# Optimization experiments

Measured on AMD Instinct MI355X. Metric: run time of the kernel, lower is better.

## Reference

```python
import jax, jax.numpy as jnp
import numpy as np

N = 4_194_304        # total nodes in the batch
NUM_GRAPHS = 32_768  # number of graphs (segments)
VOCAB = 100          # Embedding(100, 1)

# Wigner-3j contraction constants (real basis)
C01 = float(1.0 / np.sqrt(3.0))   # 0e x 1e -> 1e and 1e x 0e -> 1e
C11 = float(1.0 / np.sqrt(6.0))   # 1e x 1e -> 1e (Levi-Civita / sqrt(6))
# path weights: sqrt(ir_out.dim / fan_in_paths); 3 paths -> 1.0, 2 paths -> sqrt(3/2)
PW1 = 1.0
PW2 = float(np.sqrt(1.5))


def setup_inputs() -> dict:
    key = jax.random.key(0)
    ks = jax.random.split(key, 12)
    z = jax.random.randint(ks[0], (N,), 0, VOCAB, dtype=jnp.int32)
    pos = jax.random.normal(ks[1], (N, 3), dtype=jnp.float32)
    batch = jnp.sort(jax.random.randint(ks[2], (N,), 0, NUM_GRAPHS, dtype=jnp.int32))
    embed_table = jax.random.normal(ks[3], (VOCAB, 1), dtype=jnp.float32)
    lin_w = jax.random.normal(ks[4], (3, 3), dtype=jnp.float32) / np.sqrt(3.0)
    lin_b = jax.random.normal(ks[5], (3,), dtype=jnp.float32) * 0.1
    tp1_w = jax.random.normal(ks[6], (3,), dtype=jnp.float32)   # 3 CG paths
    tp2_w = jax.random.normal(ks[7], (2,), dtype=jnp.float32)   # 2 CG paths
    tp3_w = jax.random.normal(ks[8], (2,), dtype=jnp.float32)
    gate_w = jax.random.normal(ks[9], (2,), dtype=jnp.float32)
    fc_w = jax.random.normal(ks[10], (3, 3), dtype=jnp.float32) / np.sqrt(3.0)
    fc_b = jax.random.normal(ks[11], (3,), dtype=jnp.float32) * 0.1
    return {"z": z, "pos": pos, "batch": batch, "embed_table": embed_table,
            "lin_w": lin_w, "lin_b": lin_b, "tp1_w": tp1_w, "tp2_w": tp2_w,
            "tp3_w": tp3_w, "gate_w": gate_w, "fc_w": fc_w, "fc_b": fc_b}


def reference(z, pos, batch, embed_table, lin_w, lin_b, tp1_w, tp2_w, tp3_w, gate_w, fc_w, fc_b):
    # node features: x = [scalar embedding s (0e), transformed position v (1e)]
    s = embed_table[z][:, 0]                      # [N]
    v = pos @ lin_w.T + lin_b                     # [N, 3]
    sv = s[:, None] * v                           # [N, 3]

    # layer 1: FullyConnectedTP(x, x -> 1e); paths (0e,1e), (1e,0e), (1e,1e)
    # note: cross(v, v) == 0 structurally, kept for faithfulness to the module
    out = PW1 * (tp1_w[0] * C01 * sv
                 + tp1_w[1] * C01 * sv
                 + tp1_w[2] * C11 * jnp.cross(v, v))

    # layers 2, 3 and gate: FullyConnectedTP(out (1e), x (0e+1e) -> 1e)
    for w in (tp2_w, tp3_w, gate_w):
        out = PW2 * (w[0] * C01 * out * s[:, None]
                     + w[1] * C11 * jnp.cross(out, v))

    out = out @ fc_w.T + fc_b                     # [N, 3]
    return jax.ops.segment_sum(out, batch, num_segments=NUM_GRAPHS)  # [G, 3]
```

## Files before the change

### kernel.cpp

```cpp
#include <hip/hip_runtime.h>

#define BLOCK 256
#define NPT 8
#define CHUNK (BLOCK * NPT)
#define TBL 64

__global__ __launch_bounds__(BLOCK) void e3nn_one(
    const int* __restrict__ z, const float* __restrict__ pos,
    const int* __restrict__ batch, const float* __restrict__ embed,
    const float* __restrict__ lin_w, const float* __restrict__ lin_b,
    const float* __restrict__ tp1_w, const float* __restrict__ tp2_w,
    const float* __restrict__ tp3_w, const float* __restrict__ gate_w,
    const float* __restrict__ fc_w, const float* __restrict__ fc_b,
    float* __restrict__ out, int n, int G)
{
    __shared__ float t4[100];
    __shared__ float acc[TBL * 5];

    const int tid  = threadIdx.x;
    const int lane = tid & 63;
    const int b    = blockIdx.x;
    const int s    = b * CHUNK;
    const int e    = min(s + CHUNK, n);

    if (tid < 100) { float v = embed[tid]; float v2 = v * v; t4[tid] = v2 * v2; }
    for (int i = tid; i < TBL * 5; i += BLOCK) acc[i] = 0.f;
    __syncthreads();

    const int prev   = (s == 0) ? -1 : batch[s - 1];
    const int mylast = batch[e - 1];

    const long long i0 = (long long)s + (long long)tid * NPT;
    float px[NPT], py[NPT], pz[NPT];
    int zi[NPT], bi[NPT];

    if (i0 + NPT <= (long long)n) {
        const float4* p4 = (const float4*)(pos + i0 * 3);
        float4 q0 = p4[0], q1 = p4[1], q2 = p4[2], q3 = p4[3], q4 = p4[4], q5 = p4[5];
        px[0]=q0.x; py[0]=q0.y; pz[0]=q0.z;
        px[1]=q0.w; py[1]=q1.x; pz[1]=q1.y;
        px[2]=q1.z; py[2]=q1.w; pz[2]=q2.x;
        px[3]=q2.y; py[3]=q2.z; pz[3]=q2.w;
        px[4]=q3.x; py[4]=q3.y; pz[4]=q3.z;
        px[5]=q3.w; py[5]=q4.x; pz[5]=q4.y;
        px[6]=q4.z; py[6]=q4.w; pz[6]=q5.x;
        px[7]=q5.y; py[7]=q5.z; pz[7]=q5.w;
        int4 za = *(const int4*)(z + i0), zb = *(const int4*)(z + i0 + 4);
        zi[0]=za.x; zi[1]=za.y; zi[2]=za.z; zi[3]=za.w;
        zi[4]=zb.x; zi[5]=zb.y; zi[6]=zb.z; zi[7]=zb.w;
        int4 ba = *(const int4*)(batch + i0), bb = *(const int4*)(batch + i0 + 4);
        bi[0]=ba.x; bi[1]=ba.y; bi[2]=ba.z; bi[3]=ba.w;
        bi[4]=bb.x; bi[5]=bb.y; bi[6]=bb.z; bi[7]=bb.w;
    } else {
#pragma unroll
        for (int k = 0; k < NPT; ++k) {
            long long i = i0 + k;
            if (i < (long long)n) {
                px[k]=pos[i*3]; py[k]=pos[i*3+1]; pz[k]=pos[i*3+2];
                zi[k]=z[i]; bi[k]=batch[i];
            } else { px[k]=0.f; py[k]=0.f; pz[k]=0.f; zi[k]=0; bi[k]=-1; }
        }
    }

    auto lflush = [&](int g, float ax, float ay, float az, float at, float ac) {
        int slot = g - prev - 1;
        if (slot >= 0 && slot < TBL) {
            atomicAdd(&acc[slot*5+0], ax);
            atomicAdd(&acc[slot*5+1], ay);
            atomicAdd(&acc[slot*5+2], az);
            atomicAdd(&acc[slot*5+3], at);
            atomicAdd(&acc[slot*5+4], ac);
        }
    };

    float ax=0.f, ay=0.f, az=0.f, at=0.f, ac=0.f;
    int rb = -1;
#pragma unroll
    for (int k = 0; k < NPT; ++k) {
        if (bi[k] < 0) continue;
        float t = t4[zi[k]];
        if (bi[k] == rb) {
            ax += t*px[k]; ay += t*py[k]; az += t*pz[k]; at += t; ac += 1.f;
        } else {
            if (rb >= 0) lflush(rb, ax, ay, az, at, ac);
            rb = bi[k];
            ax = t*px[k]; ay = t*py[k]; az = t*pz[k]; at = t; ac = 1.f;
        }
    }

#pragma unroll
    for (int off = 1; off < 64; off <<= 1) {
        int   ob = __shfl_down(rb, off);
        float qx = __shfl_down(ax, off);
        float qy = __shfl_down(ay, off);
        float qz = __shfl_down(az, off);
        float qt = __shfl_down(at, off);
        float qc = __shfl_down(ac, off);
        if ((lane + off) < 64 && ob == rb) {
            ax += qx; ay += qy; az += qz; at += qt; ac += qc;
        }
    }
    {
        int pb = __shfl_up(rb, 1);
        bool head = (lane == 0) || (pb != rb);
        if (rb >= 0 && head) lflush(rb, ax, ay, az, at, ac);
    }

    if ((tid >> 6) == 3 && e < n && mylast > prev) {
        float sx=0.f, sy=0.f, sz=0.f, st=0.f, sc=0.f;
        int base = e;
        for (;;) {
            bool allok = true;
#pragma unroll
            for (int k = 0; k < 4; ++k) {
                int idx = base + lane * 4 + k;
                bool ok = (idx < n) && (batch[idx] == mylast);
                if (ok) {
                    float t = t4[z[idx]];
                    sx += t*pos[3*idx]; sy += t*pos[3*idx+1]; sz += t*pos[3*idx+2];
                    st += t; sc += 1.f;
                } else allok = false;
            }
            unsigned long long m = __ballot(allok);
            if (m != ~0ULL) break;
            base += 256;
        }
#pragma unroll
        for (int off = 1; off < 64; off <<= 1) {
            sx += __shfl_xor(sx, off);
            sy += __shfl_xor(sy, off);
            sz += __shfl_xor(sz, off);
            st += __shfl_xor(st, off);
            sc += __shfl_xor(sc, off);
        }
        if (lane == 0) {
            int slot = mylast - prev - 1;
            if (slot < TBL) {
                atomicAdd(&acc[slot*5+0], sx);
                atomicAdd(&acc[slot*5+1], sy);
                atomicAdd(&acc[slot*5+2], sz);
                atomicAdd(&acc[slot*5+3], st);
                atomicAdd(&acc[slot*5+4], sc);
            }
        }
    }

    __syncthreads();

    const float C01 = 0.57735026918962576f;
    const float PW2 = 1.2247448713915890f;
    const float k1  = (tp1_w[0] + tp1_w[1]) * C01;
    const float C   = k1 * (PW2*tp2_w[0]*C01) * (PW2*tp3_w[0]*C01) * (PW2*gate_w[0]*C01);

    float lw[9], fw[9], lbv[3], fbv[3];
#pragma unroll
    for (int i = 0; i < 9; ++i) { lw[i] = lin_w[i]; fw[i] = fc_w[i]; }
#pragma unroll
    for (int i = 0; i < 3; ++i) { lbv[i] = lin_b[i]; fbv[i] = fc_b[i]; }

    float W[9], u[3];
#pragma unroll
    for (int r = 0; r < 3; ++r) {
#pragma unroll
        for (int cc = 0; cc < 3; ++cc)
            W[r*3+cc] = fw[r*3+0]*lw[0*3+cc] + fw[r*3+1]*lw[1*3+cc] + fw[r*3+2]*lw[2*3+cc];
        u[r] = fw[r*3+0]*lbv[0] + fw[r*3+1]*lbv[1] + fw[r*3+2]*lbv[2];
    }

    const int gend  = (e == n) ? (G - 1) : mylast;
    const int count = gend - prev;

    for (int o = tid; o < count; o += BLOCK) {
        float vx=0.f, vy=0.f, vz=0.f, vt=0.f, vc=0.f;
        if (o < TBL) {
            vx = acc[o*5+0]; vy = acc[o*5+1]; vz = acc[o*5+2];
            vt = acc[o*5+3]; vc = acc[o*5+4];
        }
        int g = prev + 1 + o;
        out[3*g+0] = C * (W[0]*vx + W[1]*vy + W[2]*vz + vt*u[0]) + vc*fbv[0];
        out[3*g+1] = C * (W[3]*vx + W[4]*vy + W[5]*vz + vt*u[1]) + vc*fbv[1];
        out[3*g+2] = C * (W[6]*vx + W[7]*vy + W[8]*vz + vt*u[2]) + vc*fbv[2];
    }
}

extern "C" void kernel_launch(void* const* d_in, const int* in_sizes, int n_in,
                              void* d_out, int out_size, void* d_ws, size_t ws_size,
                              hipStream_t stream) {
    const int*   z     = (const int*)  d_in[0];
    const float* pos   = (const float*)d_in[1];
    const int*   batch = (const int*)  d_in[2];
    const float* embed = (const float*)d_in[3];
    const float* lin_w = (const float*)d_in[4];
    const float* lin_b = (const float*)d_in[5];
    const float* tp1_w = (const float*)d_in[6];
    const float* tp2_w = (const float*)d_in[7];
    const float* tp3_w = (const float*)d_in[8];
    const float* gate_w= (const float*)d_in[9];
    const float* fc_w  = (const float*)d_in[10];
    const float* fc_b  = (const float*)d_in[11];
    float* out = (float*)d_out;

    int n = in_sizes[0];
    int G = out_size / 3;

    int nblocks = (n + CHUNK - 1) / CHUNK;
    e3nn_one<<<nblocks, BLOCK, 0, stream>>>(
        z, pos, batch, embed, lin_w, lin_b,
        tp1_w, tp2_w, tp3_w, gate_w, fc_w, fc_b, out, n, G);
}
```

Before: 22.54 us.

## Stage node loads through padded shared memory for fully coalesced global reads

Full chunks now load pos, z and batch with lane-contiguous float4/int4 reads (stride across threads) and transpose them through a bank-padded shared-memory buffer, so each thread still gets its 8 consecutive nodes. The embedding lookup t4[z] is done during staging, and the global loads are issued before the table/accumulator init to overlap latency. The aim is to replace the per-thread strided 96-byte vector loads with coalesced accesses. In exchange it adds about 25KB of shared memory per block (lower occupancy) and three extra barriers.

```diff
diff --git a/kernel.cpp b/kernel.cpp
--- a/kernel.cpp
+++ b/kernel.cpp
@@ -4,6 +4,8 @@
 #define NPT 8
 #define CHUNK (BLOCK * NPT)
 #define TBL 64
+
+__device__ __forceinline__ int padw(int w) { return w + (w >> 5); }
 
 __global__ __launch_bounds__(BLOCK) void e3nn_one(
     const int* __restrict__ z, const float* __restrict__ pos,
@@ -14,8 +16,9 @@
     const float* __restrict__ fc_w, const float* __restrict__ fc_b,
     float* __restrict__ out, int n, int G)
 {
-    __shared__ float t4[100];
+    __shared__ float t4s[100];
     __shared__ float acc[TBL * 5];
+    __shared__ float stage[6336];
 
     const int tid  = threadIdx.x;
     const int lane = tid & 63;
@@ -23,42 +26,89 @@
     const int s    = b * CHUNK;
     const int e    = min(s + CHUNK, n);
 
-    if (tid < 100) { float v = embed[tid]; float v2 = v * v; t4[tid] = v2 * v2; }
-    for (int i = tid; i < TBL * 5; i += BLOCK) acc[i] = 0.f;
-    __syncthreads();
-
     const int prev   = (s == 0) ? -1 : batch[s - 1];
     const int mylast = batch[e - 1];
 
-    const long long i0 = (long long)s + (long long)tid * NPT;
-    float px[NPT], py[NPT], pz[NPT];
-    int zi[NPT], bi[NPT];
-
-    if (i0 + NPT <= (long long)n) {
-        const float4* p4 = (const float4*)(pos + i0 * 3);
-        float4 q0 = p4[0], q1 = p4[1], q2 = p4[2], q3 = p4[3], q4 = p4[4], q5 = p4[5];
-        px[0]=q0.x; py[0]=q0.y; pz[0]=q0.z;
-        px[1]=q0.w; py[1]=q1.x; pz[1]=q1.y;
-        px[2]=q1.z; py[2]=q1.w; pz[2]=q2.x;
-        px[3]=q2.y; py[3]=q2.z; pz[3]=q2.w;
-        px[4]=q3.x; py[4]=q3.y; pz[4]=q3.z;
-        px[5]=q3.w; py[5]=q4.x; pz[5]=q4.y;
-        px[6]=q4.z; py[6]=q4.w; pz[6]=q5.x;
-        px[7]=q5.y; py[7]=q5.z; pz[7]=q5.w;
-        int4 za = *(const int4*)(z + i0), zb = *(const int4*)(z + i0 + 4);
-        zi[0]=za.x; zi[1]=za.y; zi[2]=za.z; zi[3]=za.w;
-        zi[4]=zb.x; zi[5]=zb.y; zi[6]=zb.z; zi[7]=zb.w;
-        int4 ba = *(const int4*)(batch + i0), bb = *(const int4*)(batch + i0 + 4);
-        bi[0]=ba.x; bi[1]=ba.y; bi[2]=ba.z; bi[3]=ba.w;
-        bi[4]=bb.x; bi[5]=bb.y; bi[6]=bb.z; bi[7]=bb.w;
+    float px[NPT], py[NPT], pz[NPT], tv[NPT];
+    int bi[NPT];
+
+    if (e - s == CHUNK) {
+        const float4* posf4 = (const float4*)pos;
+        const int4*   z4p   = (const int4*)z;
+        const int4*   b4p   = (const int4*)batch;
+        const int F0 = b * 1536;
+        const int Z0 = b * 512;
+
+        float4 pv[6];
+#pragma unroll
+        for (int j = 0; j < 6; ++j) pv[j] = posf4[F0 + tid + 256 * j];
+        int4 zv0 = z4p[Z0 + tid], zv1 = z4p[Z0 + tid + 256];
+        int4 bv0 = b4p[Z0 + tid], bv1 = b4p[Z0 + tid + 256];
+
+        if (tid < 100) { float v = embed[tid]; float v2 = v * v; t4s[tid] = v2 * v2; }
+        for (int i2 = tid; i2 < TBL * 5; i2 += BLOCK) acc[i2] = 0.f;
+
+#pragma unroll
+        for (int j = 0; j < 6; ++j) {
+            int p0 = padw(4 * (tid + 256 * j));
+            stage[p0    ] = pv[j].x;
+            stage[p0 + 1] = pv[j].y;
+            stage[p0 + 2] = pv[j].z;
+            stage[p0 + 3] = pv[j].w;
+        }
+        __syncthreads();
+
+#pragma unroll
+        for (int k = 0; k < NPT; ++k) {
+            int w = 24 * tid + 3 * k;
+            px[k] = stage[padw(w)];
+            py[k] = stage[padw(w + 1)];
+            pz[k] = stage[padw(w + 2)];
+        }
+        __syncthreads();
+
+        {
+            int p0 = padw(4 * tid);
+            stage[p0    ] = t4s[zv0.x];
+            stage[p0 + 1] = t4s[zv0.y];
+            stage[p0 + 2] = t4s[zv0.z];
+            stage[p0 + 3] = t4s[zv0.w];
+            int p1 = padw(4 * (tid + 256));
+            stage[p1    ] = t4s[zv1.x];
+            stage[p1 + 1] = t4s[zv1.y];
+            stage[p1 + 2] = t4s[zv1.z];
+            stage[p1 + 3] = t4s[zv1.w];
+            int q0 = 2112 + p0;
+            stage[q0    ] = __int_as_float(bv0.x);
+            stage[q0 + 1] = __int_as_float(bv0.y);
+            stage[q0 + 2] = __int_as_float(bv0.z);
+            stage[q0 + 3] = __int_as_float(bv0.w);
+            int q1 = 2112 + p1;
+            stage[q1    ] = __int_as_float(bv1.x);
+            stage[q1 + 1] = __int_as_float(bv1.y);
+            stage[q1 + 2] = __int_as_float(bv1.z);
+            stage[q1 + 3] = __int_as_float(bv1.w);
+        }
+        __syncthreads();
+
+#pragma unroll
+        for (int k = 0; k < NPT; ++k) {
+            int w = 8 * tid + k;
+            tv[k] = stage[padw(w)];
+            bi[k] = __float_as_int(stage[2112 + padw(w)]);
+        }
     } else {
+        if (tid < 100) { float v = embed[tid]; float v2 = v * v; t4s[tid] = v2 * v2; }
+        for (int i2 = tid; i2 < TBL * 5; i2 += BLOCK) acc[i2] = 0.f;
+        __syncthreads();
+        long long i0 = (long long)s + (long long)tid * NPT;
 #pragma unroll
         for (int k = 0; k < NPT; ++k) {
             long long i = i0 + k;
-            if (i < (long long)n) {
-                px[k]=pos[i*3]; py[k]=pos[i*3+1]; pz[k]=pos[i*3+2];
-                zi[k]=z[i]; bi[k]=batch[i];
-            } else { px[k]=0.f; py[k]=0.f; pz[k]=0.f; zi[k]=0; bi[k]=-1; }
+            if (i < (long long)e) {
+                px[k] = pos[i*3]; py[k] = pos[i*3+1]; pz[k] = pos[i*3+2];
+                tv[k] = t4s[z[i]]; bi[k] = batch[i];
+            } else { px[k]=0.f; py[k]=0.f; pz[k]=0.f; tv[k]=0.f; bi[k] = -1; }
         }
     }
 
@@ -78,7 +128,7 @@
 #pragma unroll
     for (int k = 0; k < NPT; ++k) {
         if (bi[k] < 0) continue;
-        float t = t4[zi[k]];
+        float t = tv[k];
         if (bi[k] == rb) {
             ax += t*px[k]; ay += t*py[k]; az += t*pz[k]; at += t; ac += 1.f;
         } else {
@@ -116,7 +166,7 @@
                 int idx = base + lane * 4 + k;
                 bool ok = (idx < n) && (batch[idx] == mylast);
                 if (ok) {
-                    float t = t4[z[idx]];
+                    float t = t4s[z[idx]];
                     sx += t*pos[3*idx]; sy += t*pos[3*idx+1]; sz += t*pos[3*idx+2];
                     st += t; sc += 1.f;
                 } else allok = false;
```

Measured after the change: 26.94 us. 19.5% more time.
